# Performance work log

Measured on AMD Instinct MI355X. Metric: run time of the kernel, lower is better.

## Reference

```python
import jax, jax.numpy as jnp
import numpy as np

MU = 0            # smeared direction (init arg dir)
IS_ODD = False    # init arg is_odd -> update the EVEN subset
DIMS = (24, 24, 24, 24)
N_PLAQ = 6
PI_2 = 0.6366197723675814  # 2/pi, as in scale_coeff


def setup_inputs() -> dict:
    key = jax.random.key(0)
    k1, k2, k3 = jax.random.split(key, 3)
    shape = (4,) + DIMS + (3, 3)  # [dir, T, Z, Y, X, 3, 3]
    x_re = jax.random.normal(k1, shape, jnp.float32)
    x_im = jax.random.normal(k2, shape, jnp.float32)
    coeff = jax.random.uniform(k3, (N_PLAQ,), jnp.float32)
    return {"x_re": x_re, "x_im": x_im, "coeff": coeff}


def _adj(m):
    return jnp.conj(jnp.swapaxes(m, -1, -2))


def _shift(a, nu, n):
    # lattice .shift(nu, n): value at site + n*nu_hat (periodic); lattice axes are the leading 4
    return jnp.roll(a, -n, axis=nu)


def _eo_filter(dims, is_odd, dtype):
    # evenodd_mask % 2; filter is 1 on the UPDATED subset (odd if is_odd else even)
    grids = jnp.meshgrid(*[jnp.arange(d) for d in dims], indexing='ij')
    parity = sum(grids) % 2
    mask = parity if is_odd else 1 - parity
    return mask.astype(dtype)[..., None, None]


def _matexp(Z, terms=12, squarings=4):
    # scaling-and-squaring Taylor (Horner) matrix exponential, batched over leading dims
    Z = Z * jnp.asarray(0.5 ** squarings, dtype=jnp.float32).astype(Z.dtype)
    eye = jnp.eye(Z.shape[-1], dtype=Z.dtype)
    E = eye
    for k in range(terms, 0, -1):
        E = eye + (Z @ E) / k
    for _ in range(squarings):
        E = E @ E
    return E


def reference(x_re, x_im, coeff):
    x = (x_re + 1j * x_im).astype(jnp.complex64)  # [4, T, Z, Y, X, 3, 3]
    filt = _eo_filter(DIMS, IS_ODD, jnp.complex64)
    # filter_fixed_update: mask mu-links; staples built from fixed-subset x[mu]
    xmu_fix = x[MU] * (1.0 - filt)
    xupd = x[MU] * filt
    # scale_coeff(coeff, 0.75) = (2/pi)*0.75*atan(coeff)
    c = (PI_2 * 0.75) * jnp.arctan(coeff)
    cc = c.astype(jnp.complex64)
    # plaquette staples (n_plaq = 6 loops)
    loops = []
    for nu in range(4):
        if nu == MU:
            continue
        Umu = _shift(xmu_fix, nu, 1)      # x[mu].shift(nu, 1)
        Unu = _shift(x[nu], MU, 1)        # x[nu].shift(mu, 1)
        R = Umu @ _adj(Unu)
        stf = x[nu] @ R                   # forward staple
        L = _adj(x[nu]) @ xmu_fix
        stu = L @ Unu
        loops.append(stf)
        loops.append(_shift(stu, nu, -1)) # backward staple
    f = loops[0] * cc[0]
    for i in range(1, N_PLAQ):
        f = f + loops[i] * cc[i]
    f = f / N_PLAQ
    # stout update on the updated subset: Z = projectTangent(f @ xupd^dag); U' = exp(Z) @ U
    M = f @ _adj(xupd)
    A = 0.5 * (M - _adj(M))               # anti-hermitian part
    tr = jnp.trace(A, axis1=-2, axis2=-1)
    Zt = A - (tr / 3.0)[..., None, None] * jnp.eye(3, dtype=A.dtype)  # traceless
    E = _matexp(Zt)
    ymu = E @ xupd + xmu_fix              # combine updated and fixed subsets
    y = x.at[MU].set(ymu)
    # return real/imag stacked so output is real-valued: [4, T, Z, Y, X, 3, 3, 2]
    return jnp.stack((jnp.real(y), jnp.imag(y)), axis=-1)
```

## Files before the change

### kernel.cpp

```cpp
#include <hip/hip_runtime.h>
#include <cstdint>

#define LT 24
#define NSITE (LT*LT*LT*LT)

struct C3 { float re[9]; float im[9]; };

__device__ __forceinline__ void load9(float* d, const float* __restrict__ p) {
    float4 a, b;
    __builtin_memcpy(&a, p,     16);
    __builtin_memcpy(&b, p + 4, 16);
    d[0]=a.x; d[1]=a.y; d[2]=a.z; d[3]=a.w;
    d[4]=b.x; d[5]=b.y; d[6]=b.z; d[7]=b.w;
    d[8]=p[8];
}

__device__ __forceinline__ void loadM(C3& m, const float* __restrict__ re,
                                      const float* __restrict__ im, int off) {
    load9(m.re, re + off);
    load9(m.im, im + off);
}

__device__ __forceinline__ void storeM(float2* __restrict__ out, int cbase, const C3& m) {
    float4 v;
    v.x=m.re[0]; v.y=m.im[0]; v.z=m.re[1]; v.w=m.im[1];
    __builtin_memcpy(out + cbase,     &v, 16);
    v.x=m.re[2]; v.y=m.im[2]; v.z=m.re[3]; v.w=m.im[3];
    __builtin_memcpy(out + cbase + 2, &v, 16);
    v.x=m.re[4]; v.y=m.im[4]; v.z=m.re[5]; v.w=m.im[5];
    __builtin_memcpy(out + cbase + 4, &v, 16);
    v.x=m.re[6]; v.y=m.im[6]; v.z=m.re[7]; v.w=m.im[7];
    __builtin_memcpy(out + cbase + 6, &v, 16);
    float2 w; w.x=m.re[8]; w.y=m.im[8];
    out[cbase + 8] = w;
}

__device__ __forceinline__ void mmul(C3& o, const C3& a, const C3& b) {
#pragma unroll
    for (int r = 0; r < 3; ++r) {
#pragma unroll
        for (int c = 0; c < 3; ++c) {
            float sr = 0.f, si = 0.f;
#pragma unroll
            for (int k = 0; k < 3; ++k) {
                float ar = a.re[r*3+k], ai = a.im[r*3+k];
                float br = b.re[k*3+c], bi = b.im[k*3+c];
                sr += ar*br - ai*bi;
                si += ar*bi + ai*br;
            }
            o.re[r*3+c] = sr; o.im[r*3+c] = si;
        }
    }
}

__device__ __forceinline__ void mmul_acc(C3& f, const C3& a, const C3& b, float cr) {
#pragma unroll
    for (int r = 0; r < 3; ++r) {
#pragma unroll
        for (int c = 0; c < 3; ++c) {
            float sr = 0.f, si = 0.f;
#pragma unroll
            for (int k = 0; k < 3; ++k) {
                float ar = a.re[r*3+k], ai = a.im[r*3+k];
                float br = b.re[k*3+c], bi = b.im[k*3+c];
                sr += ar*br - ai*bi;
                si += ar*bi + ai*br;
            }
            f.re[r*3+c] += cr * sr; f.im[r*3+c] += cr * si;
        }
    }
}

__device__ __forceinline__ void mmul_adjB(C3& o, const C3& a, const C3& b) {
#pragma unroll
    for (int r = 0; r < 3; ++r) {
#pragma unroll
        for (int c = 0; c < 3; ++c) {
            float sr = 0.f, si = 0.f;
#pragma unroll
            for (int k = 0; k < 3; ++k) {
                float ar = a.re[r*3+k], ai = a.im[r*3+k];
                float br = b.re[c*3+k], bi = b.im[c*3+k];
                sr += ar*br + ai*bi;
                si += ai*br - ar*bi;
            }
            o.re[r*3+c] = sr; o.im[r*3+c] = si;
        }
    }
}

__device__ __forceinline__ void madjA_mul(C3& o, const C3& a, const C3& b) {
#pragma unroll
    for (int r = 0; r < 3; ++r) {
#pragma unroll
        for (int c = 0; c < 3; ++c) {
            float sr = 0.f, si = 0.f;
#pragma unroll
            for (int k = 0; k < 3; ++k) {
                float ar = a.re[k*3+r], ai = a.im[k*3+r];
                float br = b.re[k*3+c], bi = b.im[k*3+c];
                sr += ar*br + ai*bi;
                si += ar*bi - ai*br;
            }
            o.re[r*3+c] = sr; o.im[r*3+c] = si;
        }
    }
}

__device__ __forceinline__ int site_from_idx(int idx, int parity,
                                             int& t, int& z, int& y, int& x) {
    int xh = idx % 12;  int r = idx / 12;
    y = r % LT; r /= LT;
    z = r % LT; t = r / LT;
    x = 2 * xh + ((t + z + y + parity) & 1);
    return ((t * LT + z) * LT + y) * LT + x;
}

__global__ __launch_bounds__(256)
void stout_fused(const float* __restrict__ xre, const float* __restrict__ xim,
                 const float* __restrict__ coeff, float2* __restrict__ out) {
    const int tau = threadIdx.x;
    const bool heavy = (tau < 128);
    const int idx = blockIdx.x * 128 + (heavy ? tau : tau - 128);

    if (!heavy) {
        int t, z, y, x;
        const int s = site_from_idx(idx, 1, t, z, y, x);
        C3 m;
#pragma unroll
        for (int d = 0; d < 4; ++d) {
            const int off = (d * NSITE + s) * 9;
            loadM(m, xre, xim, off);
            storeM(out, off, m);
        }
        return;
    }

    int t, z, y, x;
    const int s = site_from_idx(idx, 0, t, z, y, x);

    float c[6];
#pragma unroll
    for (int i = 0; i < 6; ++i)
        c[i] = 0.07957747154594768f * atanf(coeff[i]);

    int tp = (t + 1 < LT) ? t + 1 : 0;
    int zp = (z + 1 < LT) ? z + 1 : 0;  int zm = (z > 0) ? z - 1 : LT - 1;
    int yp = (y + 1 < LT) ? y + 1 : 0;  int ym = (y > 0) ? y - 1 : LT - 1;
    int xp = (x + 1 < LT) ? x + 1 : 0;  int xm = (x > 0) ? x - 1 : LT - 1;

    const int stt = ((tp * LT + z) * LT + y) * LT + x;
    const int spv[3]  = { ((t  * LT + zp) * LT + y ) * LT + x,
                          ((t  * LT + z ) * LT + yp) * LT + x,
                          ((t  * LT + z ) * LT + y ) * LT + xp };
    const int smv[3]  = { ((t  * LT + zm) * LT + y ) * LT + x,
                          ((t  * LT + z ) * LT + ym) * LT + x,
                          ((t  * LT + z ) * LT + y ) * LT + xm };
    const int smtv[3] = { ((tp * LT + zm) * LT + y ) * LT + x,
                          ((tp * LT + z ) * LT + ym) * LT + x,
                          ((tp * LT + z ) * LT + y ) * LT + xm };

    C3 f;
#pragma unroll
    for (int j = 0; j < 9; ++j) { f.re[j] = 0.f; f.im[j] = 0.f; }

    C3 A, B, Cm, tmp;
#pragma unroll
    for (int i = 0; i < 3; ++i) {
        const int d = i + 1;
        loadM(A, xre, xim, (d * NSITE + s) * 9);
        storeM(out, (d * NSITE + s) * 9, A);
        loadM(B,  xre, xim, (     spv[i])        * 9);
        loadM(Cm, xre, xim, (d * NSITE + stt)    * 9);
        mmul_adjB(tmp, B, Cm);
        mmul_acc(f, A, tmp, c[2 * i]);
        loadM(A,  xre, xim, (d * NSITE + smv[i]) * 9);
        loadM(B,  xre, xim, (     smv[i])        * 9);
        loadM(Cm, xre, xim, (d * NSITE + smtv[i])* 9);
        madjA_mul(tmp, A, B);
        mmul_acc(f, tmp, Cm, c[2 * i + 1]);
    }

    C3 U;
    loadM(U, xre, xim, s * 9);

    C3 Mm;
    mmul_adjB(Mm, f, U);
    C3 Zt;
#pragma unroll
    for (int r = 0; r < 3; ++r) {
#pragma unroll
        for (int cq = 0; cq < 3; ++cq) {
            Zt.re[r*3+cq] = 0.5f * (Mm.re[r*3+cq] - Mm.re[cq*3+r]);
            Zt.im[r*3+cq] = 0.5f * (Mm.im[r*3+cq] + Mm.im[cq*3+r]);
        }
    }
    float trIm = (Zt.im[0] + Zt.im[4] + Zt.im[8]) / 3.0f;
    Zt.im[0] -= trIm; Zt.im[4] -= trIm; Zt.im[8] -= trIm;

#pragma unroll
    for (int j = 0; j < 9; ++j) { Zt.re[j] *= 0.0625f; Zt.im[j] *= 0.0625f; }

    C3 E;
#pragma unroll
    for (int j = 0; j < 9; ++j) { E.re[j] = 0.f; E.im[j] = 0.f; }
    E.re[0] = 1.f; E.re[4] = 1.f; E.re[8] = 1.f;

    C3 Tm;
#pragma unroll
    for (int k = 12; k >= 1; --k) {
        mmul(Tm, Zt, E);
        const float invk = 1.0f / (float)k;
#pragma unroll
        for (int j = 0; j < 9; ++j) {
            E.re[j] = Tm.re[j] * invk;
            E.im[j] = Tm.im[j] * invk;
        }
        E.re[0] += 1.f; E.re[4] += 1.f; E.re[8] += 1.f;
    }
#pragma unroll
    for (int q = 0; q < 4; ++q) {
        mmul(Tm, E, E);
        E = Tm;
    }

    C3 Y;
    mmul(Y, E, U);
    storeM(out, s * 9, Y);
}

extern "C" void kernel_launch(void* const* d_in, const int* in_sizes, int n_in,
                              void* d_out, int out_size, void* d_ws, size_t ws_size,
                              hipStream_t stream) {
    const float* xre   = (const float*)d_in[0];
    const float* xim   = (const float*)d_in[1];
    const float* coeff = (const float*)d_in[2];

    const int nblocks = (NSITE / 2) / 128;
    stout_fused<<<nblocks, 256, 0, stream>>>(xre, xim, coeff, (float2*)d_out);
}
```

Baseline: 247.7 us.

## Merge copy threads into heavy threads with coalesced nontemporal streaming copy

Drops the split of 128 heavy and 128 copy threads per block. Each thread now computes one even site, copies one odd mu-link, and streams directions 1-3 as a flat coalesced copy, taking float2 pairs of re/im and writing interleaved float4 with nontemporal stores. The copy is interleaved with the staple computation so its memory traffic overlaps the math, and blocks shrink to 64 threads with launch_bounds occupancy hint 3. The risk is higher register pressure, since each thread carries both the copy and the compute, and the change in occupancy.

Result: slower. 327.1 us (+32.1%).

```diff
diff --git a/kernel.cpp b/kernel.cpp
--- a/kernel.cpp
+++ b/kernel.cpp
@@ -3,6 +3,14 @@
 
 #define LT 24
 #define NSITE (LT*LT*LT*LT)
+#define HALF  (NSITE/2)
+#define NCOMPLEX (4*NSITE*9)
+
+#define BS   64
+#define NBLK (HALF/BS)
+#define Q0D  (NSITE*9/2)
+
+typedef float vf4 __attribute__((ext_vector_type(4)));
 
 struct C3 { float re[9]; float im[9]; };
 
@@ -116,33 +124,27 @@
     return ((t * LT + z) * LT + y) * LT + x;
 }
 
-__global__ __launch_bounds__(256)
-void stout_fused(const float* __restrict__ xre, const float* __restrict__ xim,
-                 const float* __restrict__ coeff, float2* __restrict__ out) {
-    const int tau = threadIdx.x;
-    const bool heavy = (tau < 128);
-    const int idx = blockIdx.x * 128 + (heavy ? tau : tau - 128);
-
-    if (!heavy) {
-        int t, z, y, x;
-        const int s = site_from_idx(idx, 1, t, z, y, x);
-        C3 m;
-#pragma unroll
-        for (int d = 0; d < 4; ++d) {
-            const int off = (d * NSITE + s) * 9;
-            loadM(m, xre, xim, off);
-            storeM(out, off, m);
-        }
-        return;
-    }
-
-    int t, z, y, x;
-    const int s = site_from_idx(idx, 0, t, z, y, x);
+__global__ __launch_bounds__(BS, 3)
+void stout_all(const float* __restrict__ xre, const float* __restrict__ xim,
+               const float* __restrict__ coeff, float2* __restrict__ out) {
+    const int tidg = blockIdx.x * BS + threadIdx.x;
+
+    const float2* __restrict__ re2 = (const float2*)xre;
+    const float2* __restrict__ im2 = (const float2*)xim;
+    vf4* __restrict__ o4 = (vf4*)out;
+
+    int t1, z1, y1, x1;
+    const int s1 = site_from_idx(tidg, 1, t1, z1, y1, x1);
+    C3 modd;
+    loadM(modd, xre, xim, s1 * 9);
 
     float c[6];
 #pragma unroll
     for (int i = 0; i < 6; ++i)
         c[i] = 0.07957747154594768f * atanf(coeff[i]);
+
+    int t, z, y, x;
+    const int s = site_from_idx(tidg, 0, t, z, y, x);
 
     int tp = (t + 1 < LT) ? t + 1 : 0;
     int zp = (z + 1 < LT) ? z + 1 : 0;  int zm = (z > 0) ? z - 1 : LT - 1;
@@ -160,6 +162,8 @@
                           ((tp * LT + z ) * LT + ym) * LT + x,
                           ((tp * LT + z ) * LT + y ) * LT + xm };
 
+    storeM(out, s1 * 9, modd);
+
     C3 f;
 #pragma unroll
     for (int j = 0; j < 9; ++j) { f.re[j] = 0.f; f.im[j] = 0.f; }
@@ -169,16 +173,24 @@
     for (int i = 0; i < 3; ++i) {
         const int d = i + 1;
         loadM(A, xre, xim, (d * NSITE + s) * 9);
-        storeM(out, (d * NSITE + s) * 9, A);
         loadM(B,  xre, xim, (     spv[i])        * 9);
         loadM(Cm, xre, xim, (d * NSITE + stt)    * 9);
         mmul_adjB(tmp, B, Cm);
         mmul_acc(f, A, tmp, c[2 * i]);
         loadM(A,  xre, xim, (d * NSITE + smv[i]) * 9);
         loadM(B,  xre, xim, (     smv[i])        * 9);
+        madjA_mul(tmp, A, B);
         loadM(Cm, xre, xim, (d * NSITE + smtv[i])* 9);
-        madjA_mul(tmp, A, B);
         mmul_acc(f, tmp, Cm, c[2 * i + 1]);
+
+#pragma unroll
+        for (int j = 0; j < 9; ++j) {
+            const int q = Q0D + (i * 9 + j) * HALF + tidg;
+            float2 r  = re2[q];
+            float2 im = im2[q];
+            vf4 o = { r.x, im.x, r.y, im.y };
+            __builtin_nontemporal_store(o, o4 + q);
+        }
     }
 
     C3 U;
@@ -236,6 +248,5 @@
     const float* xim   = (const float*)d_in[1];
     const float* coeff = (const float*)d_in[2];
 
-    const int nblocks = (NSITE / 2) / 128;
-    stout_fused<<<nblocks, 256, 0, stream>>>(xre, xim, coeff, (float2*)d_out);
-}
+    stout_all<<<NBLK, BS, 0, stream>>>(xre, xim, coeff, (float2*)d_out);
+}
```
